# Performance work log

Measured on AMD Instinct MI355X. Metric: run time of the kernel, lower is better.

Reference implementation:

```python
import jax, jax.numpy as jnp
import numpy as np

N = 1024
DIM = 128
HEADS = 8
DK = DIM // HEADS
EDIM = 16
EPS = 1e-5
NEG = -10000.0


def _lin(k, din, dout):
    return jax.random.normal(k, (din, dout), jnp.float32) * (1.0 / np.sqrt(din))


def setup_inputs() -> dict:
    key = jax.random.key(0)
    ks = jax.random.split(key, 10)
    mask = jax.random.randint(ks[2], (N, N), 0, 2).astype(bool)
    mask = mask | jnp.eye(N, dtype=bool)  # self-loops always valid
    return {
        "x": jax.random.normal(ks[0], (N, DIM), jnp.float32),
        "edge_feat": jax.random.normal(ks[1], (N, N, EDIM), jnp.float32),
        "mask": mask,
        "Wq": _lin(ks[3], DIM, DIM), "bq": jnp.zeros((DIM,), jnp.float32),
        "Wk": _lin(ks[4], DIM, DIM), "bk": jnp.zeros((DIM,), jnp.float32),
        "Wv": _lin(ks[5], DIM, DIM), "bv": jnp.zeros((DIM,), jnp.float32),
        "Wae": _lin(ks[6], EDIM, HEADS), "bae": jnp.zeros((HEADS,), jnp.float32),
        "Wve": _lin(ks[7], EDIM, DIM), "bve": jnp.zeros((DIM,), jnp.float32),
        "Wo": _lin(ks[8], DIM, DIM), "bo": jnp.zeros((DIM,), jnp.float32),
        "gamma": jnp.ones((DIM,), jnp.float32),
        "beta": jnp.zeros((DIM,), jnp.float32),
    }


def reference(x, edge_feat, mask, Wq, bq, Wk, bk, Wv, bv, Wae, bae, Wve, bve, Wo, bo, gamma, beta):
    n, dim = x.shape
    heads = bae.shape[0]
    dk = dim // heads
    # pre-LayerNorm
    mu = jnp.mean(x, axis=-1, keepdims=True)
    var = jnp.mean(jnp.square(x - mu), axis=-1, keepdims=True)
    h = (x - mu) * jax.lax.rsqrt(var + EPS) * gamma + beta
    q = (h @ Wq + bq).reshape(n, heads, dk)
    k = (h @ Wk + bk).reshape(n, heads, dk)
    v = (h @ Wv + bv).reshape(n, heads, dk)
    # attention logits with per-edge additive bias: (n, m, heads)
    att = jnp.einsum('nhd,mhd->nmh', q, k) / np.sqrt(dk).astype(np.float32)
    att = att + edge_feat @ Wae + bae
    att = jnp.where(mask[..., None], att, NEG)
    alpha = jax.nn.softmax(att, axis=1)  # softmax over source nodes m
    # edge-conditioned values: msg_{nm} = v_m + U(e_{nm})
    edge_val = (edge_feat @ Wve + bve).reshape(n, n, heads, dk)
    out = jnp.einsum('nmh,mhd->nhd', alpha, v) + jnp.einsum('nmh,nmhd->nhd', alpha, edge_val)
    out = out.reshape(n, dim) @ Wo + bo
    return x + out
```

## Files before the change

### kernel.cpp

```cpp
#include <hip/hip_runtime.h>
#include <hip/hip_bf16.h>

#define NNODE 1024
#define DIM 128
#define HEADS 8
#define DK 16
#define EDIM 16
#define BN 8
#define MR 16
#define NCH 8
#define NGRP 8
#define KV_ROW 160
#define H_STRIDE 20
#define EF_ROW 20
#define EF_NSTR 324
#define MK_STR 17
#define LOG2E 1.44269504f

#define SMEM_F 8448
#define KV_OFF 2592
#define MK_OFF 7712

__global__ __launch_bounds__(384)
void ln_qkv_kernel(const float* __restrict__ x,
                   const float* __restrict__ Wq, const float* __restrict__ bq,
                   const float* __restrict__ Wk, const float* __restrict__ bk,
                   const float* __restrict__ Wv, const float* __restrict__ bv,
                   const float* __restrict__ gamma, const float* __restrict__ beta,
                   float* __restrict__ qg, float* __restrict__ kg, float* __restrict__ vg) {
    const int n = blockIdx.x;
    const int t = threadIdx.x;
    __shared__ float hrow[DIM];
    __shared__ float part[4];

    float xv = 0.f;
    if (t < 128) {
        xv = x[n * DIM + t];
        float v = xv;
        #pragma unroll
        for (int off = 32; off >= 1; off >>= 1) v += __shfl_xor(v, off);
        if ((t & 63) == 0) part[t >> 6] = v;
    }
    __syncthreads();
    const float mu = (part[0] + part[1]) * (1.0f / DIM);
    const float dx = xv - mu;
    if (t < 128) {
        float v = dx * dx;
        #pragma unroll
        for (int off = 32; off >= 1; off >>= 1) v += __shfl_xor(v, off);
        if ((t & 63) == 0) part[2 + (t >> 6)] = v;
    }
    __syncthreads();
    if (t < 128) {
        const float var = (part[2] + part[3]) * (1.0f / DIM);
        hrow[t] = dx * rsqrtf(var + 1e-5f) * gamma[t] + beta[t];
    }
    __syncthreads();

    const int which = t >> 7;
    const int col = t & 127;
    const float* W = (which == 0) ? Wq : (which == 1) ? Wk : Wv;
    const float* b = (which == 0) ? bq : (which == 1) ? bk : bv;
    float* o       = (which == 0) ? qg : (which == 1) ? kg : vg;
    float a0 = b[col], a1 = 0.f;
    #pragma unroll 8
    for (int i = 0; i < DIM; i += 2) {
        a0 = fmaf(hrow[i],     W[i * DIM + col],       a0);
        a1 = fmaf(hrow[i + 1], W[(i + 1) * DIM + col], a1);
    }
    o[n * DIM + col] = a0 + a1;
}

__global__ __launch_bounds__(256, 2)
void attn_kernel(const float* __restrict__ qg, const float* __restrict__ kg,
                 const float* __restrict__ vg, const float* __restrict__ ef,
                 const int* __restrict__ mask,
                 const float* __restrict__ Wae, const float* __restrict__ bae,
                 float* __restrict__ acc) {
    const int t = threadIdx.x;
    const int s  = t >> 5;
    const int np = (t >> 3) & 3;
    const int h  = t & 7;
    const int wid = t >> 6, lane = t & 63;
    const int bx = blockIdx.x;
    const int n0  = (bx >> 3) * BN;
    const int grp = bx & 7;
    const int mb0 = grp * (MR * NCH);

    __shared__ float smem[SMEM_F];
    float* ef_lds = smem;
    float* k_lds  = smem + KV_OFF;
    float* v_lds  = smem + KV_OFF + MR * KV_ROW;
    int*   mk_lds = (int*)(smem + MK_OFF);

    float qreg[2][DK];
    #pragma unroll
    for (int hf = 0; hf < 2; ++hf) {
        const float* qp = qg + (size_t)(n0 + np + 4 * hf) * DIM + h * DK;
        #pragma unroll
        for (int d4 = 0; d4 < 4; ++d4) {
            const float4 qv = *(const float4*)(qp + d4 * 4);
            qreg[hf][d4 * 4 + 0] = qv.x; qreg[hf][d4 * 4 + 1] = qv.y;
            qreg[hf][d4 * 4 + 2] = qv.z; qreg[hf][d4 * 4 + 3] = qv.w;
        }
    }
    float waec[EDIM];
    #pragma unroll
    for (int e = 0; e < EDIM; ++e) waec[e] = Wae[e * HEADS + h] * LOG2E;
    const float baeh = bae[h] * LOG2E;

    float sl[2] = {0.f, 0.f};
    float accv[2][DK], accT[2][EDIM];
    #pragma unroll
    for (int hf = 0; hf < 2; ++hf) {
        #pragma unroll
        for (int d = 0; d < DK; ++d) accv[hf][d] = 0.f;
        #pragma unroll
        for (int e = 0; e < EDIM; ++e) accT[hf][e] = 0.f;
    }

    #pragma unroll 1
    for (int c = 0; c < NCH; ++c) {
        const int mb = mb0 + c * MR;
        if (c) __syncthreads();

        #pragma unroll
        for (int r = 0; r < 2; ++r) {
            const int idx = t + 256 * r;
            const int nn = idx >> 6;
            const int mm = (idx >> 2) & 15;
            const int q4 = idx & 3;
            const float4 ev = *(const float4*)(ef + ((size_t)(n0 + nn) * NNODE + mb + mm) * EDIM + q4 * 4);
            *(float4*)&ef_lds[nn * EF_NSTR + mm * EF_ROW + q4 * 4] = ev;
        }
        #pragma unroll
        for (int r = 0; r < 2; ++r) {
            const int idx = t + 256 * r;
            const int mm = idx >> 5, c4 = idx & 31;
            const int hh = c4 >> 2, d4 = c4 & 3;
            const float4 kq = *(const float4*)(kg + (size_t)(mb + mm) * DIM + c4 * 4);
            const float4 vq = *(const float4*)(vg + (size_t)(mb + mm) * DIM + c4 * 4);
            *(float4*)&k_lds[mm * KV_ROW + hh * H_STRIDE + d4 * 4] = kq;
            *(float4*)&v_lds[mm * KV_ROW + hh * H_STRIDE + d4 * 4] = vq;
        }
        if (t < BN * MR) {
            const int nn = t >> 4, mm = t & 15;
            mk_lds[nn * MK_STR + mm] = mask[(size_t)(n0 + nn) * NNODE + (mb + mm)];
        }
        __syncthreads();

        #pragma unroll
        for (int j = 0; j < 2; ++j) {
            const int m = j * 8 + s;
            float kk[DK], vv[DK];
            const float* kp = &k_lds[m * KV_ROW + h * H_STRIDE];
            const float* vp = &v_lds[m * KV_ROW + h * H_STRIDE];
            #pragma unroll
            for (int d4 = 0; d4 < 4; ++d4) {
                const float4 k4 = *(const float4*)(kp + d4 * 4);
                kk[d4 * 4 + 0] = k4.x; kk[d4 * 4 + 1] = k4.y;
                kk[d4 * 4 + 2] = k4.z; kk[d4 * 4 + 3] = k4.w;
                const float4 v4 = *(const float4*)(vp + d4 * 4);
                vv[d4 * 4 + 0] = v4.x; vv[d4 * 4 + 1] = v4.y;
                vv[d4 * 4 + 2] = v4.z; vv[d4 * 4 + 3] = v4.w;
            }
            #pragma unroll
            for (int hf = 0; hf < 2; ++hf) {
                const int n = np + 4 * hf;
                const float* ep = &ef_lds[n * EF_NSTR + m * EF_ROW];
                float efv[EDIM];
                #pragma unroll
                for (int e4 = 0; e4 < 4; ++e4) {
                    const float4 ev = *(const float4*)(ep + e4 * 4);
                    efv[e4 * 4 + 0] = ev.x; efv[e4 * 4 + 1] = ev.y;
                    efv[e4 * 4 + 2] = ev.z; efv[e4 * 4 + 3] = ev.w;
                }
                float bias = baeh, dot = 0.f;
                #pragma unroll
                for (int e = 0; e < EDIM; ++e) bias = fmaf(efv[e], waec[e], bias);
                #pragma unroll
                for (int d = 0; d < DK; ++d) dot = fmaf(qreg[hf][d], kk[d], dot);
                const float lg = fmaf(dot, 0.25f * LOG2E, bias);
                const float p = mk_lds[n * MK_STR + m] ? __builtin_amdgcn_exp2f(lg) : 0.f;
                sl[hf] += p;
                #pragma unroll
                for (int d = 0; d < DK; ++d) accv[hf][d] = fmaf(p, vv[d], accv[hf][d]);
                #pragma unroll
                for (int e = 0; e < EDIM; ++e) accT[hf][e] = fmaf(p, efv[e], accT[hf][e]);
            }
        }
    }

    #pragma unroll
    for (int hf = 0; hf < 2; ++hf) {
        sl[hf] += __shfl_xor(sl[hf], 32);
        #pragma unroll
        for (int d = 0; d < DK; ++d) accv[hf][d] += __shfl_xor(accv[hf][d], 32);
        #pragma unroll
        for (int e = 0; e < EDIM; ++e) accT[hf][e] += __shfl_xor(accT[hf][e], 32);
    }
    __syncthreads();
    float* red = smem;
    if (lane < 32) {
        float* rp = &red[((wid * 4 + np) * 8 + h) * 66];
        #pragma unroll
        for (int hf = 0; hf < 2; ++hf) {
            rp[hf * 33 + 0] = sl[hf];
            #pragma unroll
            for (int d = 0; d < DK; ++d) rp[hf * 33 + 1 + d] = accv[hf][d];
            #pragma unroll
            for (int e = 0; e < EDIM; ++e) rp[hf * 33 + 17 + e] = accT[hf][e];
        }
    }
    __syncthreads();
    for (int v = t; v < BN * HEADS * 33; v += 256) {
        const int n = v / 264;
        const int rem = v - n * 264;
        const int hh = rem / 33;
        const int idx = rem - hh * 33;
        const int nnp = n & 3, hf = n >> 2;
        float sum = 0.f;
        #pragma unroll
        for (int w = 0; w < 4; ++w)
            sum += red[((w * 4 + nnp) * 8 + hh) * 66 + hf * 33 + idx];
        acc[((size_t)(n0 + n) * NGRP + grp) * 264 + rem] = sum;
    }
}

__global__ __launch_bounds__(128)
void final_kernel(const float* __restrict__ acc,
                  const float* __restrict__ Wve, const float* __restrict__ bve,
                  const float* __restrict__ x,
                  const float* __restrict__ Wo, const float* __restrict__ bo,
                  float* __restrict__ out) {
    const int n = blockIdx.x, t = threadIdx.x;
    __shared__ float ab[HEADS * 33];
    __shared__ float orow[DIM];
    const float* ap = acc + (size_t)n * NGRP * 264;
    for (int u = t; u < HEADS * 33; u += 128) {
        float sv = 0.f;
        #pragma unroll
        for (int g = 0; g < NGRP; ++g) sv += ap[g * 264 + u];
        ab[u] = sv;
    }
    __syncthreads();
    const int col = t, hh = col >> 4, dd = col & 15;
    const float slv = ab[hh * 33];
    float acc2 = 0.f;
    #pragma unroll
    for (int e = 0; e < EDIM; ++e) acc2 = fmaf(ab[hh * 33 + 17 + e], Wve[e * DIM + col], acc2);
    orow[col] = (ab[hh * 33 + 1 + dd] + acc2) / slv + bve[col];
    __syncthreads();
    float o0 = bo[col] + x[(size_t)n * DIM + col], o1 = 0.f;
    #pragma unroll 8
    for (int i = 0; i < DIM; i += 2) {
        o0 = fmaf(orow[i],     Wo[i * DIM + col],       o0);
        o1 = fmaf(orow[i + 1], Wo[(i + 1) * DIM + col], o1);
    }
    out[(size_t)n * DIM + col] = o0 + o1;
}

extern "C" void kernel_launch(void* const* d_in, const int* in_sizes, int n_in,
                              void* d_out, int out_size, void* d_ws, size_t ws_size,
                              hipStream_t stream) {
    const float* x     = (const float*)d_in[0];
    const float* ef    = (const float*)d_in[1];
    const int*   mask  = (const int*)d_in[2];
    const float* Wq    = (const float*)d_in[3];
    const float* bq    = (const float*)d_in[4];
    const float* Wk    = (const float*)d_in[5];
    const float* bk    = (const float*)d_in[6];
    const float* Wv    = (const float*)d_in[7];
    const float* bv    = (const float*)d_in[8];
    const float* Wae   = (const float*)d_in[9];
    const float* bae   = (const float*)d_in[10];
    const float* Wve   = (const float*)d_in[11];
    const float* bve   = (const float*)d_in[12];
    const float* Wo    = (const float*)d_in[13];
    const float* bo    = (const float*)d_in[14];
    const float* gamma = (const float*)d_in[15];
    const float* beta  = (const float*)d_in[16];

    float* ws = (float*)d_ws;
    float* accb = ws;
    float* qg   = ws + (size_t)NNODE * NGRP * 264;
    float* kg   = qg + (size_t)NNODE * DIM;
    float* vg   = kg + (size_t)NNODE * DIM;

    ln_qkv_kernel<<<NNODE, 384, 0, stream>>>(x, Wq, bq, Wk, bk, Wv, bv, gamma, beta, qg, kg, vg);
    attn_kernel<<<(NNODE / BN) * NGRP, 256, 0, stream>>>(qg, kg, vg, ef, mask, Wae, bae, accb);
    final_kernel<<<NNODE, 128, 0, stream>>>(accb, Wve, bve, x, Wo, bo, (float*)d_out);
}
```

Measured before the change: 178.6 us.

## Double-buffer LDS tiles with register prefetch of next chunk in attention loop

Splits shared memory into two buffers and loads the next chunk's edge features, K, V and mask into registers before computing the current chunk, then writes them into the alternate buffer. This overlaps global-memory latency with compute and removes one barrier per iteration. In exchange it roughly doubles LDS usage and adds 6 float4 plus an int of live registers, which may reduce occupancy under the 2-blocks-per-SM launch bound.

```diff
diff --git a/kernel.cpp b/kernel.cpp
--- a/kernel.cpp
+++ b/kernel.cpp
@@ -17,7 +17,8 @@
 #define MK_STR 17
 #define LOG2E 1.44269504f
 
-#define SMEM_F 8448
+#define BUF 7848
+#define SMEM_F (2 * BUF)
 #define KV_OFF 2592
 #define MK_OFF 7712
 
@@ -88,10 +89,6 @@
     const int mb0 = grp * (MR * NCH);
 
     __shared__ float smem[SMEM_F];
-    float* ef_lds = smem;
-    float* k_lds  = smem + KV_OFF;
-    float* v_lds  = smem + KV_OFF + MR * KV_ROW;
-    int*   mk_lds = (int*)(smem + MK_OFF);
 
     float qreg[2][DK];
     #pragma unroll
@@ -119,19 +116,18 @@
         for (int e = 0; e < EDIM; ++e) accT[hf][e] = 0.f;
     }
 
-    #pragma unroll 1
-    for (int c = 0; c < NCH; ++c) {
-        const int mb = mb0 + c * MR;
-        if (c) __syncthreads();
-
+    {
+        const int mb = mb0;
+        float* ef_n = smem;
+        float* k_n  = smem + KV_OFF;
+        float* v_n  = k_n + MR * KV_ROW;
+        int*   mk_n = (int*)(smem + MK_OFF);
         #pragma unroll
         for (int r = 0; r < 2; ++r) {
             const int idx = t + 256 * r;
-            const int nn = idx >> 6;
-            const int mm = (idx >> 2) & 15;
-            const int q4 = idx & 3;
+            const int nn = idx >> 6, mm = (idx >> 2) & 15, q4 = idx & 3;
             const float4 ev = *(const float4*)(ef + ((size_t)(n0 + nn) * NNODE + mb + mm) * EDIM + q4 * 4);
-            *(float4*)&ef_lds[nn * EF_NSTR + mm * EF_ROW + q4 * 4] = ev;
+            *(float4*)&ef_n[nn * EF_NSTR + mm * EF_ROW + q4 * 4] = ev;
         }
         #pragma unroll
         for (int r = 0; r < 2; ++r) {
@@ -140,21 +136,48 @@
             const int hh = c4 >> 2, d4 = c4 & 3;
             const float4 kq = *(const float4*)(kg + (size_t)(mb + mm) * DIM + c4 * 4);
             const float4 vq = *(const float4*)(vg + (size_t)(mb + mm) * DIM + c4 * 4);
-            *(float4*)&k_lds[mm * KV_ROW + hh * H_STRIDE + d4 * 4] = kq;
-            *(float4*)&v_lds[mm * KV_ROW + hh * H_STRIDE + d4 * 4] = vq;
-        }
-        if (t < BN * MR) {
-            const int nn = t >> 4, mm = t & 15;
-            mk_lds[nn * MK_STR + mm] = mask[(size_t)(n0 + nn) * NNODE + (mb + mm)];
-        }
-        __syncthreads();
+            *(float4*)&k_n[mm * KV_ROW + hh * H_STRIDE + d4 * 4] = kq;
+            *(float4*)&v_n[mm * KV_ROW + hh * H_STRIDE + d4 * 4] = vq;
+        }
+        if (t < BN * MR)
+            mk_n[(t >> 4) * MK_STR + (t & 15)] = mask[(size_t)(n0 + (t >> 4)) * NNODE + (mb + (t & 15))];
+    }
+    __syncthreads();
+
+    #pragma unroll 1
+    for (int c = 0; c < NCH; ++c) {
+        float* ef_c = smem + (c & 1) * BUF;
+        float* k_c  = ef_c + KV_OFF;
+        float* v_c  = k_c + MR * KV_ROW;
+        int*   mk_c = (int*)(ef_c + MK_OFF);
+        const bool pf = (c + 1 < NCH);
+
+        float4 nef[2], nk[2], nv[2]; int nmk = 0;
+        if (pf) {
+            const int mb = mb0 + (c + 1) * MR;
+            #pragma unroll
+            for (int r = 0; r < 2; ++r) {
+                const int idx = t + 256 * r;
+                const int nn = idx >> 6, mm = (idx >> 2) & 15, q4 = idx & 3;
+                nef[r] = *(const float4*)(ef + ((size_t)(n0 + nn) * NNODE + mb + mm) * EDIM + q4 * 4);
+            }
+            #pragma unroll
+            for (int r = 0; r < 2; ++r) {
+                const int idx = t + 256 * r;
+                const int mm = idx >> 5, c4 = idx & 31;
+                nk[r] = *(const float4*)(kg + (size_t)(mb + mm) * DIM + c4 * 4);
+                nv[r] = *(const float4*)(vg + (size_t)(mb + mm) * DIM + c4 * 4);
+            }
+            if (t < BN * MR)
+                nmk = mask[(size_t)(n0 + (t >> 4)) * NNODE + (mb + (t & 15))];
+        }
 
         #pragma unroll
         for (int j = 0; j < 2; ++j) {
             const int m = j * 8 + s;
             float kk[DK], vv[DK];
-            const float* kp = &k_lds[m * KV_ROW + h * H_STRIDE];
-            const float* vp = &v_lds[m * KV_ROW + h * H_STRIDE];
+            const float* kp = &k_c[m * KV_ROW + h * H_STRIDE];
+            const float* vp = &v_c[m * KV_ROW + h * H_STRIDE];
             #pragma unroll
             for (int d4 = 0; d4 < 4; ++d4) {
                 const float4 k4 = *(const float4*)(kp + d4 * 4);
@@ -167,7 +190,7 @@
             #pragma unroll
             for (int hf = 0; hf < 2; ++hf) {
                 const int n = np + 4 * hf;
-                const float* ep = &ef_lds[n * EF_NSTR + m * EF_ROW];
+                const float* ep = &ef_c[n * EF_NSTR + m * EF_ROW];
                 float efv[EDIM];
                 #pragma unroll
                 for (int e4 = 0; e4 < 4; ++e4) {
@@ -181,7 +204,7 @@
                 #pragma unroll
                 for (int d = 0; d < DK; ++d) dot = fmaf(qreg[hf][d], kk[d], dot);
                 const float lg = fmaf(dot, 0.25f * LOG2E, bias);
-                const float p = mk_lds[n * MK_STR + m] ? __builtin_amdgcn_exp2f(lg) : 0.f;
+                const float p = mk_c[n * MK_STR + m] ? __builtin_amdgcn_exp2f(lg) : 0.f;
                 sl[hf] += p;
                 #pragma unroll
                 for (int d = 0; d < DK; ++d) accv[hf][d] = fmaf(p, vv[d], accv[hf][d]);
@@ -189,6 +212,30 @@
                 for (int e = 0; e < EDIM; ++e) accT[hf][e] = fmaf(p, efv[e], accT[hf][e]);
             }
         }
+
+        if (pf) {
+            float* ef_n = smem + ((c + 1) & 1) * BUF;
+            float* k_n  = ef_n + KV_OFF;
+            float* v_n  = k_n + MR * KV_ROW;
+            int*   mk_n = (int*)(ef_n + MK_OFF);
+            #pragma unroll
+            for (int r = 0; r < 2; ++r) {
+                const int idx = t + 256 * r;
+                const int nn = idx >> 6, mm = (idx >> 2) & 15, q4 = idx & 3;
+                *(float4*)&ef_n[nn * EF_NSTR + mm * EF_ROW + q4 * 4] = nef[r];
+            }
+            #pragma unroll
+            for (int r = 0; r < 2; ++r) {
+                const int idx = t + 256 * r;
+                const int mm = idx >> 5, c4 = idx & 31;
+                const int hh = c4 >> 2, d4 = c4 & 3;
+                *(float4*)&k_n[mm * KV_ROW + hh * H_STRIDE + d4 * 4] = nk[r];
+                *(float4*)&v_n[mm * KV_ROW + hh * H_STRIDE + d4 * 4] = nv[r];
+            }
+            if (t < BN * MR)
+                mk_n[(t >> 4) * MK_STR + (t & 15)] = nmk;
+        }
+        __syncthreads();
     }
 
     #pragma unroll
@@ -199,7 +246,6 @@
         #pragma unroll
         for (int e = 0; e < EDIM; ++e) accT[hf][e] += __shfl_xor(accT[hf][e], 32);
     }
-    __syncthreads();
     float* red = smem;
     if (lane < 32) {
         float* rp = &red[((wid * 4 + np) * 8 + h) * 66];
```

New measurement: 257.6 us. 1.44x slower.

## Give each wavefront a private LDS slice to drop block-wide barriers in attention loop

Applied to the files above, without the earlier changes.

Each of the four wavefronts now owns a contiguous 32-node source range and stages its own K/V, edge-feature and mask tiles into a private LDS region. It processes 4 source rows per chunk, so the per-chunk __syncthreads is no longer needed. Global loads are issued into registers before the LDS stores, giving some load overlap. The risk is that visibility between lanes of the same wavefront now relies on wave-synchronous execution with no explicit barrier, and there are more, smaller chunks, which adds loop and load overhead.

```diff
diff --git a/kernel.cpp b/kernel.cpp
--- a/kernel.cpp
+++ b/kernel.cpp
@@ -7,19 +7,18 @@
 #define DK 16
 #define EDIM 16
 #define BN 8
-#define MR 16
-#define NCH 8
 #define NGRP 8
 #define KV_ROW 160
 #define H_STRIDE 20
 #define EF_ROW 20
-#define EF_NSTR 324
-#define MK_STR 17
+#define EFW_NSTR 104
 #define LOG2E 1.44269504f
 
-#define SMEM_F 8448
-#define KV_OFF 2592
-#define MK_OFF 7712
+#define WREG 2176
+#define VW_OFF 640
+#define EFW_OFF 1280
+#define MKW_OFF 2112
+#define SMEM_F (4 * WREG)
 
 __global__ __launch_bounds__(384)
 void ln_qkv_kernel(const float* __restrict__ x,
@@ -78,20 +77,21 @@
                  const float* __restrict__ Wae, const float* __restrict__ bae,
                  float* __restrict__ acc) {
     const int t = threadIdx.x;
-    const int s  = t >> 5;
-    const int np = (t >> 3) & 3;
-    const int h  = t & 7;
-    const int wid = t >> 6, lane = t & 63;
+    const int lane = t & 63;
+    const int wid = t >> 6;
+    const int sp = lane >> 5;
+    const int np = (lane >> 3) & 3;
+    const int h  = lane & 7;
     const int bx = blockIdx.x;
     const int n0  = (bx >> 3) * BN;
     const int grp = bx & 7;
-    const int mb0 = grp * (MR * NCH);
+    const int mb_w = grp * 128 + wid * 32;
 
     __shared__ float smem[SMEM_F];
-    float* ef_lds = smem;
-    float* k_lds  = smem + KV_OFF;
-    float* v_lds  = smem + KV_OFF + MR * KV_ROW;
-    int*   mk_lds = (int*)(smem + MK_OFF);
+    float* k_w  = smem + wid * WREG;
+    float* v_w  = k_w + VW_OFF;
+    float* ef_w = k_w + EFW_OFF;
+    int*   mk_w = (int*)(k_w + MKW_OFF);
 
     float qreg[2][DK];
     #pragma unroll
@@ -120,41 +120,50 @@
     }
 
     #pragma unroll 1
-    for (int c = 0; c < NCH; ++c) {
-        const int mb = mb0 + c * MR;
-        if (c) __syncthreads();
-
+    for (int c = 0; c < 8; ++c) {
+        const int mb = mb_w + c * 4;
+
+        const int kvrow = sp * 2 + (np >> 1);
+        const int kvc4  = (np & 1) * 16 + (h << 1);
+        float4 kq[2], vq[2], ev[2]; int mki = 0;
         #pragma unroll
         for (int r = 0; r < 2; ++r) {
-            const int idx = t + 256 * r;
-            const int nn = idx >> 6;
-            const int mm = (idx >> 2) & 15;
-            const int q4 = idx & 3;
-            const float4 ev = *(const float4*)(ef + ((size_t)(n0 + nn) * NNODE + mb + mm) * EDIM + q4 * 4);
-            *(float4*)&ef_lds[nn * EF_NSTR + mm * EF_ROW + q4 * 4] = ev;
+            const int idx = r * 64 + lane;
+            const int row = idx >> 5, c4 = idx & 31;
+            kq[r] = *(const float4*)(kg + (size_t)(mb + row) * DIM + c4 * 4);
+            vq[r] = *(const float4*)(vg + (size_t)(mb + row) * DIM + c4 * 4);
         }
         #pragma unroll
         for (int r = 0; r < 2; ++r) {
-            const int idx = t + 256 * r;
-            const int mm = idx >> 5, c4 = idx & 31;
+            const int idx = r * 64 + lane;
+            const int nn = idx >> 4, mm = (idx >> 2) & 3, q4 = idx & 3;
+            ev[r] = *(const float4*)(ef + ((size_t)(n0 + nn) * NNODE + mb + mm) * EDIM + q4 * 4);
+        }
+        if (lane < 32)
+            mki = mask[(size_t)(n0 + (lane >> 2)) * NNODE + (mb + (lane & 3))];
+        #pragma unroll
+        for (int r = 0; r < 2; ++r) {
+            const int idx = r * 64 + lane;
+            const int row = idx >> 5, c4 = idx & 31;
             const int hh = c4 >> 2, d4 = c4 & 3;
-            const float4 kq = *(const float4*)(kg + (size_t)(mb + mm) * DIM + c4 * 4);
-            const float4 vq = *(const float4*)(vg + (size_t)(mb + mm) * DIM + c4 * 4);
-            *(float4*)&k_lds[mm * KV_ROW + hh * H_STRIDE + d4 * 4] = kq;
-            *(float4*)&v_lds[mm * KV_ROW + hh * H_STRIDE + d4 * 4] = vq;
-        }
-        if (t < BN * MR) {
-            const int nn = t >> 4, mm = t & 15;
-            mk_lds[nn * MK_STR + mm] = mask[(size_t)(n0 + nn) * NNODE + (mb + mm)];
-        }
-        __syncthreads();
+            *(float4*)&k_w[row * KV_ROW + hh * H_STRIDE + d4 * 4] = kq[r];
+            *(float4*)&v_w[row * KV_ROW + hh * H_STRIDE + d4 * 4] = vq[r];
+        }
+        #pragma unroll
+        for (int r = 0; r < 2; ++r) {
+            const int idx = r * 64 + lane;
+            const int nn = idx >> 4, mm = (idx >> 2) & 3, q4 = idx & 3;
+            *(float4*)&ef_w[nn * EFW_NSTR + mm * EF_ROW + q4 * 4] = ev[r];
+        }
+        if (lane < 32)
+            mk_w[lane] = mki;
 
         #pragma unroll
         for (int j = 0; j < 2; ++j) {
-            const int m = j * 8 + s;
+            const int ml = sp * 2 + j;
             float kk[DK], vv[DK];
-            const float* kp = &k_lds[m * KV_ROW + h * H_STRIDE];
-            const float* vp = &v_lds[m * KV_ROW + h * H_STRIDE];
+            const float* kp = &k_w[ml * KV_ROW + h * H_STRIDE];
+            const float* vp = &v_w[ml * KV_ROW + h * H_STRIDE];
             #pragma unroll
             for (int d4 = 0; d4 < 4; ++d4) {
                 const float4 k4 = *(const float4*)(kp + d4 * 4);
@@ -167,13 +176,13 @@
             #pragma unroll
             for (int hf = 0; hf < 2; ++hf) {
                 const int n = np + 4 * hf;
-                const float* ep = &ef_lds[n * EF_NSTR + m * EF_ROW];
+                const float* ep = &ef_w[n * EFW_NSTR + ml * EF_ROW];
                 float efv[EDIM];
                 #pragma unroll
                 for (int e4 = 0; e4 < 4; ++e4) {
-                    const float4 ev = *(const float4*)(ep + e4 * 4);
-                    efv[e4 * 4 + 0] = ev.x; efv[e4 * 4 + 1] = ev.y;
-                    efv[e4 * 4 + 2] = ev.z; efv[e4 * 4 + 3] = ev.w;
+                    const float4 e4v = *(const float4*)(ep + e4 * 4);
+                    efv[e4 * 4 + 0] = e4v.x; efv[e4 * 4 + 1] = e4v.y;
+                    efv[e4 * 4 + 2] = e4v.z; efv[e4 * 4 + 3] = e4v.w;
                 }
                 float bias = baeh, dot = 0.f;
                 #pragma unroll
@@ -181,7 +190,7 @@
                 #pragma unroll
                 for (int d = 0; d < DK; ++d) dot = fmaf(qreg[hf][d], kk[d], dot);
                 const float lg = fmaf(dot, 0.25f * LOG2E, bias);
-                const float p = mk_lds[n * MK_STR + m] ? __builtin_amdgcn_exp2f(lg) : 0.f;
+                const float p = mk_w[n * 4 + ml] ? __builtin_amdgcn_exp2f(lg) : 0.f;
                 sl[hf] += p;
                 #pragma unroll
                 for (int d = 0; d < DK; ++d) accv[hf][d] = fmaf(p, vv[d], accv[hf][d]);
```

Result: faster. 172.6 us (-3.3%).
